# Kernel tuning notes

Hardware: AMD Instinct MI355X
Metric: run time of the kernel (lower is better)

The kernel has to match this reference:

```python
import jax, jax.numpy as jnp
import numpy as np

N_NODES = 100000
N_EDGES = 800000
DIMS = [(768, 64), (64, 32), (32, 16), (16, 5)]


def setup_inputs() -> dict:
    key = jax.random.key(0)
    ks = jax.random.split(key, 3 + 3 * len(DIMS))
    inp = {
        "x": jax.random.normal(ks[0], (N_NODES, DIMS[0][0]), jnp.float32),
        "edge_index": jax.random.randint(ks[1], (2, N_EDGES), 0, N_NODES),
        "edge_weight": jax.random.uniform(ks[2], (N_EDGES,), jnp.float32),
    }
    for i, (di, do) in enumerate(DIMS, start=1):
        s = 1.0 / np.sqrt(di)
        k0, k1, k2 = ks[3 * i], ks[3 * i + 1], ks[3 * i + 2]
        inp[f"W{i}l"] = jax.random.uniform(k0, (di, do), jnp.float32, -s, s)
        inp[f"W{i}r"] = jax.random.uniform(k1, (di, do), jnp.float32, -s, s)
        inp[f"b{i}"] = jax.random.uniform(k2, (do,), jnp.float32, -s, s)
    return inp


def _sage_conv(h, src, dst, inv_deg, Wl, Wr, b):
    # SAGEConv (mean aggregation): lin_l(mean_{j->i} h_j) + lin_r(h_i)
    agg = jax.ops.segment_sum(h[src], dst, num_segments=h.shape[0]) * inv_deg[:, None]
    return agg @ Wl + h @ Wr + b


def reference(x, edge_index, edge_weight,
              W1l, W1r, b1, W2l, W2r, b2, W3l, W3r, b3, W4l, W4r, b4):
    # edge_weight is accepted (matches original forward) but PyG SAGEConv mean
    # aggregation ignores it. Dropout is identity (deterministic eval reference).
    src, dst = edge_index[0], edge_index[1]
    deg = jax.ops.segment_sum(jnp.ones((src.shape[0],), x.dtype), dst,
                              num_segments=x.shape[0])
    inv_deg = jnp.where(deg > 0, 1.0 / deg, 0.0)
    h = jax.nn.relu(_sage_conv(x, src, dst, inv_deg, W1l, W1r, b1))
    h = jax.nn.relu(_sage_conv(h, src, dst, inv_deg, W2l, W2r, b2))
    h = jax.nn.relu(_sage_conv(h, src, dst, inv_deg, W3l, W3r, b3))
    return _sage_conv(h, src, dst, inv_deg, W4l, W4r, b4)
```

## Files before the change

kernel.cpp:

```cpp
#include <hip/hip_runtime.h>

using half8 = __attribute__((ext_vector_type(8))) _Float16;
using f32x4 = __attribute__((ext_vector_type(4))) float;

typedef __attribute__((address_space(3))) unsigned int lds_uint;
typedef __attribute__((address_space(1))) const unsigned int glb_uint;
__device__ __forceinline__ void async_copy16(const void* g, void* l) {
  __builtin_amdgcn_global_load_lds((glb_uint*)g, (lds_uint*)l, 16, 0, 0);
}

__device__ __forceinline__ void raw_barrier() {
  asm volatile("" ::: "memory");
  __builtin_amdgcn_s_barrier();
  asm volatile("" ::: "memory");
}

__global__ void zero_kernel(int4* __restrict__ p, int n4) {
  int i = blockIdx.x * 256 + threadIdx.x;
  if (i < n4) p[i] = make_int4(0, 0, 0, 0);
}

__global__ void prep_all_kernel(const float* __restrict__ W1l, const float* __restrict__ W1r,
                                const float* __restrict__ W2l, const float* __restrict__ W2r,
                                const float* __restrict__ W3l, const float* __restrict__ W3r,
                                const float* __restrict__ W4l, const float* __restrict__ W4r,
                                _Float16* __restrict__ w1, _Float16* __restrict__ w2,
                                _Float16* __restrict__ w3, _Float16* __restrict__ w4) {
  int i = blockIdx.x * 256 + threadIdx.x;
  if (i < 98304) {
    int c = i / 768, k = i - c * 768;
    float v = (c < 64) ? W1l[k * 64 + c] : W1r[k * 64 + (c - 64)];
    w1[i] = (_Float16)v;
  } else if (i < 98304 + 4096) {
    int j = i - 98304;
    int c = j >> 6, k = j & 63;
    float v = (c < 32) ? W2l[k * 32 + c] : W2r[k * 32 + (c - 32)];
    w2[j] = (_Float16)v;
  } else if (i < 98304 + 4096 + 1024) {
    int j = i - (98304 + 4096);
    int c = j >> 5, k = j & 31;
    float v = (c < 16) ? W3l[k * 16 + c] : W3r[k * 16 + (c - 16)];
    w3[j] = (_Float16)v;
  } else if (i < 98304 + 4096 + 1024 + 512) {
    int j = i - (98304 + 4096 + 1024);
    int c = j >> 5, k = j & 31;
    float v = 0.f;
    if (k < 16) {
      if (c < 5) v = W4l[k * 5 + c];
      else if (c < 10) v = W4r[k * 5 + (c - 5)];
    }
    w4[j] = (_Float16)v;
  }
}

__global__ void deg_kernel(const int* __restrict__ dst, int* __restrict__ cnt, int e) {
  int i = blockIdx.x * 256 + threadIdx.x;
  if (i < e) atomicAdd(&cnt[dst[i]], 1);
}

__global__ void scan1_kernel(const int* __restrict__ cnt, int* __restrict__ off,
                             int* __restrict__ bsum, float* __restrict__ invd, int nodes) {
  __shared__ int sh[256];
  int tid = threadIdx.x;
  int base = blockIdx.x * 1024 + tid * 4;
  int a0 = (base + 0 < nodes) ? cnt[base + 0] : 0;
  int a1 = (base + 1 < nodes) ? cnt[base + 1] : 0;
  int a2 = (base + 2 < nodes) ? cnt[base + 2] : 0;
  int a3 = (base + 3 < nodes) ? cnt[base + 3] : 0;
  if (base + 0 < nodes) invd[base + 0] = a0 > 0 ? 1.0f / (float)a0 : 0.f;
  if (base + 1 < nodes) invd[base + 1] = a1 > 0 ? 1.0f / (float)a1 : 0.f;
  if (base + 2 < nodes) invd[base + 2] = a2 > 0 ? 1.0f / (float)a2 : 0.f;
  if (base + 3 < nodes) invd[base + 3] = a3 > 0 ? 1.0f / (float)a3 : 0.f;
  int s3 = a0 + a1 + a2 + a3;
  sh[tid] = s3;
  __syncthreads();
  for (int d = 1; d < 256; d <<= 1) {
    int v = (tid >= d) ? sh[tid - d] : 0;
    __syncthreads();
    sh[tid] += v;
    __syncthreads();
  }
  int excl = sh[tid] - s3;
  if (base + 0 <= nodes) off[base + 0] = excl;
  if (base + 1 <= nodes) off[base + 1] = excl + a0;
  if (base + 2 <= nodes) off[base + 2] = excl + a0 + a1;
  if (base + 3 <= nodes) off[base + 3] = excl + a0 + a1 + a2;
  if (tid == 255) bsum[blockIdx.x] = sh[255];
}

__global__ void scan2_kernel(int* __restrict__ bsum, int nb) {
  __shared__ int sh[128];
  int tid = threadIdx.x;
  int v = (tid < nb) ? bsum[tid] : 0;
  sh[tid] = v;
  __syncthreads();
  for (int d = 1; d < 128; d <<= 1) {
    int u = (tid >= d) ? sh[tid - d] : 0;
    __syncthreads();
    sh[tid] += u;
    __syncthreads();
  }
  if (tid < nb) bsum[tid] = sh[tid] - v;
}

__global__ void scan3_kernel(int* __restrict__ off, const int* __restrict__ bsum, int ntot) {
  int i = blockIdx.x * 256 + threadIdx.x;
  if (i < ntot) off[i] += bsum[i >> 10];
}

__global__ void sortfill_kernel(const int* __restrict__ src, const int* __restrict__ dst,
                                const int* __restrict__ off, int* __restrict__ cur,
                                int* __restrict__ csr, int e) {
  int i = blockIdx.x * 256 + threadIdx.x;
  if (i < e) {
    int d = dst[i];
    int pos = atomicAdd(&cur[d], 1);
    csr[off[d] + pos] = src[i];
  }
}

__global__ __launch_bounds__(256, 3) void gemm1_kernel(
    const float* __restrict__ x,
    const _Float16* __restrict__ w16,
    const float* __restrict__ bias,
    _Float16* __restrict__ p, _Float16* __restrict__ q, int n) {
  constexpr int DI = 768, BK = 32, NT = DI / BK;
  __shared__ float aS[2][128 * BK];
  __shared__ _Float16 bS[2][128 * BK];
  int t = threadIdx.x;
  int lane = t & 63, w = t >> 6;
  int lm = lane & 15, lk = lane >> 4;
  int m0 = blockIdx.x * 128;

  const float* agp[4];
  int abase[4];
#pragma unroll
  for (int j = 0; j < 4; ++j) {
    int g = (j * 4 + w) * 64 + lane;
    int row = g >> 3, gi = g & 7;
    int gj = gi ^ (row & 7);
    int grow = m0 + row;
    if (grow >= n) grow = n - 1;
    agp[j] = x + (size_t)grow * DI + gj * 4;
    abase[j] = (j * 4 + w) * 256;
  }
  const _Float16* bgp[2];
  int bbase[2];
#pragma unroll
  for (int j = 0; j < 2; ++j) {
    int g = (j * 4 + w) * 64 + lane;
    int c = g >> 2, gi = g & 3;
    int gj = gi ^ ((c >> 1) & 3);
    bgp[j] = w16 + (size_t)c * DI + gj * 8;
    bbase[j] = (j * 4 + w) * 512;
  }

  f32x4 acc[2][8];
#pragma unroll
  for (int mi = 0; mi < 2; ++mi)
#pragma unroll
    for (int ni = 0; ni < 8; ++ni) acc[mi][ni] = (f32x4){0.f, 0.f, 0.f, 0.f};

  int r0l = w * 32 + lm, r1l = r0l + 16;
  int sw = lm & 7;
  int bsw = (lk ^ ((lm >> 1) & 3)) << 3;

  auto compute_tile = [&](const float* ab, const _Float16* bb) {
    f32x4 v0a = *(const f32x4*)(ab + r0l * 32 + (((lk * 2 + 0) ^ sw) << 2));
    f32x4 v0b = *(const f32x4*)(ab + r0l * 32 + (((lk * 2 + 1) ^ sw) << 2));
    f32x4 v1a = *(const f32x4*)(ab + r1l * 32 + (((lk * 2 + 0) ^ sw) << 2));
    f32x4 v1b = *(const f32x4*)(ab + r1l * 32 + (((lk * 2 + 1) ^ sw) << 2));
    half8 a0, a1;
#pragma unroll
    for (int j = 0; j < 4; ++j) {
      a0[j] = (_Float16)v0a[j]; a0[4 + j] = (_Float16)v0b[j];
      a1[j] = (_Float16)v1a[j]; a1[4 + j] = (_Float16)v1b[j];
    }
#pragma unroll
    for (int ni = 0; ni < 8; ++ni) {
      half8 b = *(const half8*)(bb + ni * 512 + lm * 32 + bsw);
      acc[0][ni] = __builtin_amdgcn_mfma_f32_16x16x32_f16(a0, b, acc[0][ni], 0, 0, 0);
      acc[1][ni] = __builtin_amdgcn_mfma_f32_16x16x32_f16(a1, b, acc[1][ni], 0, 0, 0);
    }
  };

#pragma unroll
  for (int j = 0; j < 4; ++j) async_copy16(agp[j], &aS[0][abase[j]]);
#pragma unroll
  for (int j = 0; j < 2; ++j) async_copy16(bgp[j], &bS[0][bbase[j]]);

  for (int ts = 0; ts < NT - 1; ++ts) {
    int cur = ts & 1;
    int kc = (ts + 1) * BK;
#pragma unroll
    for (int j = 0; j < 4; ++j) async_copy16(agp[j] + kc, &aS[cur ^ 1][abase[j]]);
#pragma unroll
    for (int j = 0; j < 2; ++j) async_copy16(bgp[j] + kc, &bS[cur ^ 1][bbase[j]]);
    asm volatile("s_waitcnt vmcnt(6)" ::: "memory");
    raw_barrier();
    compute_tile(aS[cur], bS[cur]);
    raw_barrier();
  }
  asm volatile("s_waitcnt vmcnt(0)" ::: "memory");
  raw_barrier();
  compute_tile(aS[(NT - 1) & 1], bS[(NT - 1) & 1]);

#pragma unroll
  for (int mi = 0; mi < 2; ++mi)
#pragma unroll
    for (int ni = 0; ni < 8; ++ni) {
      int col = ni * 16 + lm;
#pragma unroll
      for (int j = 0; j < 4; ++j) {
        int row = m0 + w * 32 + mi * 16 + lk * 4 + j;
        if (row < n) {
          float v = acc[mi][ni][j];
          if (col < 64) p[(size_t)row * 64 + col] = (_Float16)v;
          else q[(size_t)row * 64 + (col - 64)] = (_Float16)(v + bias[col - 64]);
        }
      }
    }
}

template <int DIR, int DIP, int PSI, int NC, int NCR, int DO, int PSO>
__global__ __launch_bounds__(256) void fused_agg_gemm_kernel(
    const _Float16* __restrict__ pin, const _Float16* __restrict__ qin,
    const int* __restrict__ off, const int* __restrict__ csr, const float* __restrict__ invd,
    const _Float16* __restrict__ w16, const float* __restrict__ bias,
    _Float16* __restrict__ pout, _Float16* __restrict__ qout, int n) {
  constexpr int SP = DIP + 8;
  constexpr int C8 = DIR / 8;
  constexpr int CT = C8 / 2;
  constexpr int NF = NC / 16;
  __shared__ _Float16 hs[128 * SP];
  int t = threadIdx.x;
  int node_l = t >> 1, half = t & 1;
  int node = blockIdx.x * 128 + node_l;

  if (node < n) {
    int e0 = off[node], e1 = off[node + 1];
    const half8* p8 = (const half8*)pin;
    float s[CT][8];
#pragma unroll
    for (int c = 0; c < CT; ++c)
#pragma unroll
      for (int j = 0; j < 8; ++j) s[c][j] = 0.f;
    for (int e = e0; e < e1; ++e) {
      int src = csr[e];
#pragma unroll
      for (int c = 0; c < CT; ++c) {
        half8 v = p8[(size_t)src * PSI + half * CT + c];
#pragma unroll
        for (int j = 0; j < 8; ++j) s[c][j] += (float)v[j];
      }
    }
    float id = invd[node];
#pragma unroll
    for (int c = 0; c < CT; ++c) {
      half8 qv = ((const half8*)qin)[(size_t)node * PSI + half * CT + c];
      half8 o;
#pragma unroll
      for (int j = 0; j < 8; ++j) o[j] = (_Float16)fmaxf(s[c][j] * id + (float)qv[j], 0.f);
      *(half8*)(hs + node_l * SP + (half * CT + c) * 8) = o;
    }
    if (DIP > DIR) {
      half8 z = {};
      *(half8*)(hs + node_l * SP + (C8 + half) * 8) = z;
    }
  }
  __syncthreads();

  int lane = t & 63, w = t >> 6;
  int lm = lane & 15, lk = lane >> 4;
  int r0l = w * 32 + lm, r1l = r0l + 16;
  const _Float16* wp = w16 + (size_t)lm * DIP + lk * 8;
  f32x4 acc[2][NF];
#pragma unroll
  for (int mi = 0; mi < 2; ++mi)
#pragma unroll
    for (int ni = 0; ni < NF; ++ni) acc[mi][ni] = (f32x4){0.f, 0.f, 0.f, 0.f};
#pragma unroll
  for (int kc = 0; kc < DIP; kc += 32) {
    half8 a0 = *(const half8*)(hs + r0l * SP + kc + lk * 8);
    half8 a1 = *(const half8*)(hs + r1l * SP + kc + lk * 8);
#pragma unroll
    for (int ni = 0; ni < NF; ++ni) {
      half8 b = *(const half8*)(wp + (size_t)ni * 16 * DIP + kc);
      acc[0][ni] = __builtin_amdgcn_mfma_f32_16x16x32_f16(a0, b, acc[0][ni], 0, 0, 0);
      acc[1][ni] = __builtin_amdgcn_mfma_f32_16x16x32_f16(a1, b, acc[1][ni], 0, 0, 0);
    }
  }
#pragma unroll
  for (int mi = 0; mi < 2; ++mi)
#pragma unroll
    for (int ni = 0; ni < NF; ++ni) {
      int col = ni * 16 + lm;
      if (col >= NCR) continue;
#pragma unroll
      for (int j = 0; j < 4; ++j) {
        int row = blockIdx.x * 128 + w * 32 + mi * 16 + lk * 4 + j;
        if (row < n) {
          float v = acc[mi][ni][j];
          if (col < DO) pout[(size_t)row * PSO + col] = (_Float16)v;
          else qout[(size_t)row * PSO + (col - DO)] = (_Float16)(v + bias[col - DO]);
        }
      }
    }
}

__global__ __launch_bounds__(256) void aggregate_last_kernel(
    const _Float16* __restrict__ p, const _Float16* __restrict__ q,
    const int* __restrict__ off, const int* __restrict__ csr,
    const float* __restrict__ invd, float* __restrict__ out, int n) {
  int t = blockIdx.x * 256 + threadIdx.x;
  int node = t >> 3;
  int c = t & 7;
  if (node >= n || c >= 5) return;
  int e0 = off[node], e1 = off[node + 1];
  float s = 0.f;
  for (int e = e0; e < e1; ++e) s += (float)p[(size_t)csr[e] * 8 + c];
  out[(size_t)node * 5 + c] = s * invd[node] + (float)q[(size_t)node * 8 + c];
}

extern "C" void kernel_launch(void* const* d_in, const int* in_sizes, int n_in,
                              void* d_out, int out_size, void* d_ws, size_t ws_size,
                              hipStream_t stream) {
  const float* x = (const float*)d_in[0];
  const int* ei = (const int*)d_in[1];
  const int E = in_sizes[1] / 2;
  const int* esrc = ei;
  const int* edst = ei + E;
  const float* W1l = (const float*)d_in[3];
  const float* W1r = (const float*)d_in[4];
  const float* b1 = (const float*)d_in[5];
  const float* W2l = (const float*)d_in[6];
  const float* W2r = (const float*)d_in[7];
  const float* b2 = (const float*)d_in[8];
  const float* W3l = (const float*)d_in[9];
  const float* W3r = (const float*)d_in[10];
  const float* b3 = (const float*)d_in[11];
  const float* W4l = (const float*)d_in[12];
  const float* W4r = (const float*)d_in[13];
  const float* b4 = (const float*)d_in[14];
  const int N = in_sizes[0] / 768;
  float* out = (float*)d_out;
  (void)n_in; (void)out_size; (void)ws_size;

  char* base = (char*)d_ws;
  size_t o = 0;
  auto alloc = [&](size_t bytes) -> void* {
    void* ptr = base + o;
    o = (o + bytes + 255) & ~(size_t)255;
    return ptr;
  };
  int* cnt = (int*)alloc((size_t)2 * N * 4);
  int* cur = cnt + N;
  int* off = (int*)alloc((size_t)(N + 1) * 4);
  int* bsum = (int*)alloc(1024);
  int* csr = (int*)alloc((size_t)E * 4);
  float* invd = (float*)alloc((size_t)N * 4);
  _Float16* w1 = (_Float16*)alloc((size_t)128 * 768 * 2);
  _Float16* w2 = (_Float16*)alloc((size_t)64 * 64 * 2);
  _Float16* w3 = (_Float16*)alloc((size_t)32 * 32 * 2);
  _Float16* w4 = (_Float16*)alloc((size_t)16 * 32 * 2);
  _Float16* P1 = (_Float16*)alloc((size_t)N * 64 * 2);
  _Float16* Q1 = (_Float16*)alloc((size_t)N * 64 * 2);
  _Float16* P2 = (_Float16*)alloc((size_t)N * 32 * 2);
  _Float16* Q2 = (_Float16*)alloc((size_t)N * 32 * 2);
  _Float16* P3 = (_Float16*)alloc((size_t)N * 16 * 2);
  _Float16* Q3 = (_Float16*)alloc((size_t)N * 16 * 2);
  _Float16* P4 = (_Float16*)alloc((size_t)N * 8 * 2);
  _Float16* Q4 = (_Float16*)alloc((size_t)N * 8 * 2);

  const int n4 = (2 * N + 3) / 4;
  zero_kernel<<<(n4 + 255) / 256, 256, 0, stream>>>((int4*)cnt, n4);
  prep_all_kernel<<<(98304 + 4096 + 1024 + 512 + 255) / 256, 256, 0, stream>>>(
      W1l, W1r, W2l, W2r, W3l, W3r, W4l, W4r, w1, w2, w3, w4);

  deg_kernel<<<(E + 255) / 256, 256, 0, stream>>>(edst, cnt, E);
  const int nb = (N + 1 + 1023) / 1024;
  scan1_kernel<<<nb, 256, 0, stream>>>(cnt, off, bsum, invd, N);
  scan2_kernel<<<1, 128, 0, stream>>>(bsum, nb);
  scan3_kernel<<<(N + 1 + 255) / 256, 256, 0, stream>>>(off, bsum, N + 1);
  sortfill_kernel<<<(E + 255) / 256, 256, 0, stream>>>(esrc, edst, off, cur, csr, E);

  const int gb = (N + 127) / 128;
  gemm1_kernel<<<gb, 256, 0, stream>>>(x, w1, b1, P1, Q1, N);
  fused_agg_gemm_kernel<64, 64, 8, 64, 64, 32, 32>
      <<<gb, 256, 0, stream>>>(P1, Q1, off, csr, invd, w2, b2, P2, Q2, N);
  fused_agg_gemm_kernel<32, 32, 4, 32, 32, 16, 16>
      <<<gb, 256, 0, stream>>>(P2, Q2, off, csr, invd, w3, b3, P3, Q3, N);
  fused_agg_gemm_kernel<16, 32, 2, 16, 10, 5, 8>
      <<<gb, 256, 0, stream>>>(P3, Q3, off, csr, invd, w4, b4, P4, Q4, N);
  aggregate_last_kernel<<<(N * 8 + 255) / 256, 256, 0, stream>>>(P4, Q4, off, csr, invd, out, N);
}
```

Baseline: 269.8 us.

## Widen per-node aggregation threads, unroll edge loop, fuse zeroing into prep

Fuses the counter-zeroing kernel into the weight-prep kernel to save a launch. The fused aggregate+GEMM kernels move to 512-thread blocks with four threads per node. Each wave now does one 16-row MFMA tile, and edge gathers are unrolled by two to get more loads in flight. The final aggregation uses one thread per node with vectorised half8 loads instead of eight scalar-loading threads. This trades some per-thread work and occupancy changes for more memory-level parallelism in the latency-bound gathers.

```diff
diff --git a/kernel.cpp b/kernel.cpp
--- a/kernel.cpp
+++ b/kernel.cpp
@@ -15,17 +15,13 @@
   asm volatile("" ::: "memory");
 }
 
-__global__ void zero_kernel(int4* __restrict__ p, int n4) {
-  int i = blockIdx.x * 256 + threadIdx.x;
-  if (i < n4) p[i] = make_int4(0, 0, 0, 0);
-}
-
-__global__ void prep_all_kernel(const float* __restrict__ W1l, const float* __restrict__ W1r,
-                                const float* __restrict__ W2l, const float* __restrict__ W2r,
-                                const float* __restrict__ W3l, const float* __restrict__ W3r,
-                                const float* __restrict__ W4l, const float* __restrict__ W4r,
-                                _Float16* __restrict__ w1, _Float16* __restrict__ w2,
-                                _Float16* __restrict__ w3, _Float16* __restrict__ w4) {
+__global__ void prep_zero_kernel(const float* __restrict__ W1l, const float* __restrict__ W1r,
+                                 const float* __restrict__ W2l, const float* __restrict__ W2r,
+                                 const float* __restrict__ W3l, const float* __restrict__ W3r,
+                                 const float* __restrict__ W4l, const float* __restrict__ W4r,
+                                 _Float16* __restrict__ w1, _Float16* __restrict__ w2,
+                                 _Float16* __restrict__ w3, _Float16* __restrict__ w4,
+                                 int4* __restrict__ zp, int n4) {
   int i = blockIdx.x * 256 + threadIdx.x;
   if (i < 98304) {
     int c = i / 768, k = i - c * 768;
@@ -50,6 +46,9 @@
       else if (c < 10) v = W4r[k * 5 + (c - 5)];
     }
     w4[j] = (_Float16)v;
+  } else {
+    int j = i - (98304 + 4096 + 1024 + 512);
+    if (j < n4) zp[j] = make_int4(0, 0, 0, 0);
   }
 }
 
@@ -223,103 +222,133 @@
 }
 
 template <int DIR, int DIP, int PSI, int NC, int NCR, int DO, int PSO>
-__global__ __launch_bounds__(256) void fused_agg_gemm_kernel(
+__global__ __launch_bounds__(512) void fused_agg_gemm_kernel(
     const _Float16* __restrict__ pin, const _Float16* __restrict__ qin,
     const int* __restrict__ off, const int* __restrict__ csr, const float* __restrict__ invd,
     const _Float16* __restrict__ w16, const float* __restrict__ bias,
     _Float16* __restrict__ pout, _Float16* __restrict__ qout, int n) {
   constexpr int SP = DIP + 8;
   constexpr int C8 = DIR / 8;
-  constexpr int CT = C8 / 2;
+  constexpr int ACT = (C8 >= 4) ? 4 : C8;
+  constexpr int CQ = C8 / ACT;
   constexpr int NF = NC / 16;
   __shared__ _Float16 hs[128 * SP];
   int t = threadIdx.x;
-  int node_l = t >> 1, half = t & 1;
+  int node_l = t >> 2, q4 = t & 3;
   int node = blockIdx.x * 128 + node_l;
 
   if (node < n) {
-    int e0 = off[node], e1 = off[node + 1];
-    const half8* p8 = (const half8*)pin;
-    float s[CT][8];
-#pragma unroll
-    for (int c = 0; c < CT; ++c)
-#pragma unroll
-      for (int j = 0; j < 8; ++j) s[c][j] = 0.f;
-    for (int e = e0; e < e1; ++e) {
-      int src = csr[e];
-#pragma unroll
-      for (int c = 0; c < CT; ++c) {
-        half8 v = p8[(size_t)src * PSI + half * CT + c];
-#pragma unroll
-        for (int j = 0; j < 8; ++j) s[c][j] += (float)v[j];
+    if (q4 < ACT) {
+      int e0 = off[node], e1 = off[node + 1];
+      const half8* p8 = (const half8*)pin;
+      float s[CQ][8];
+#pragma unroll
+      for (int c = 0; c < CQ; ++c)
+#pragma unroll
+        for (int j = 0; j < 8; ++j) s[c][j] = 0.f;
+      int e = e0;
+      for (; e + 2 <= e1; e += 2) {
+        int i0 = csr[e], i1 = csr[e + 1];
+        half8 v0[CQ], v1[CQ];
+#pragma unroll
+        for (int c = 0; c < CQ; ++c) v0[c] = p8[(size_t)i0 * PSI + q4 * CQ + c];
+#pragma unroll
+        for (int c = 0; c < CQ; ++c) v1[c] = p8[(size_t)i1 * PSI + q4 * CQ + c];
+#pragma unroll
+        for (int c = 0; c < CQ; ++c)
+#pragma unroll
+          for (int j = 0; j < 8; ++j) {
+            s[c][j] += (float)v0[c][j];
+            s[c][j] += (float)v1[c][j];
+          }
       }
-    }
-    float id = invd[node];
-#pragma unroll
-    for (int c = 0; c < CT; ++c) {
-      half8 qv = ((const half8*)qin)[(size_t)node * PSI + half * CT + c];
-      half8 o;
-#pragma unroll
-      for (int j = 0; j < 8; ++j) o[j] = (_Float16)fmaxf(s[c][j] * id + (float)qv[j], 0.f);
-      *(half8*)(hs + node_l * SP + (half * CT + c) * 8) = o;
-    }
-    if (DIP > DIR) {
+      if (e < e1) {
+        int i0 = csr[e];
+#pragma unroll
+        for (int c = 0; c < CQ; ++c) {
+          half8 v = p8[(size_t)i0 * PSI + q4 * CQ + c];
+#pragma unroll
+          for (int j = 0; j < 8; ++j) s[c][j] += (float)v[j];
+        }
+      }
+      float id = invd[node];
+#pragma unroll
+      for (int c = 0; c < CQ; ++c) {
+        half8 qv = ((const half8*)qin)[(size_t)node * PSI + q4 * CQ + c];
+        half8 o;
+#pragma unroll
+        for (int j = 0; j < 8; ++j) o[j] = (_Float16)fmaxf(s[c][j] * id + (float)qv[j], 0.f);
+        *(half8*)(hs + node_l * SP + (q4 * CQ + c) * 8) = o;
+      }
+    } else if (DIP > DIR && (q4 - ACT) < (DIP - DIR) / 8) {
       half8 z = {};
-      *(half8*)(hs + node_l * SP + (C8 + half) * 8) = z;
+      *(half8*)(hs + node_l * SP + (C8 + (q4 - ACT)) * 8) = z;
     }
   }
   __syncthreads();
 
   int lane = t & 63, w = t >> 6;
   int lm = lane & 15, lk = lane >> 4;
-  int r0l = w * 32 + lm, r1l = r0l + 16;
+  int row_l = w * 16 + lm;
   const _Float16* wp = w16 + (size_t)lm * DIP + lk * 8;
-  f32x4 acc[2][NF];
-#pragma unroll
-  for (int mi = 0; mi < 2; ++mi)
-#pragma unroll
-    for (int ni = 0; ni < NF; ++ni) acc[mi][ni] = (f32x4){0.f, 0.f, 0.f, 0.f};
+  f32x4 acc[NF];
+#pragma unroll
+  for (int ni = 0; ni < NF; ++ni) acc[ni] = (f32x4){0.f, 0.f, 0.f, 0.f};
 #pragma unroll
   for (int kc = 0; kc < DIP; kc += 32) {
-    half8 a0 = *(const half8*)(hs + r0l * SP + kc + lk * 8);
-    half8 a1 = *(const half8*)(hs + r1l * SP + kc + lk * 8);
+    half8 a = *(const half8*)(hs + row_l * SP + kc + lk * 8);
 #pragma unroll
     for (int ni = 0; ni < NF; ++ni) {
       half8 b = *(const half8*)(wp + (size_t)ni * 16 * DIP + kc);
-      acc[0][ni] = __builtin_amdgcn_mfma_f32_16x16x32_f16(a0, b, acc[0][ni], 0, 0, 0);
-      acc[1][ni] = __builtin_amdgcn_mfma_f32_16x16x32_f16(a1, b, acc[1][ni], 0, 0, 0);
-    }
-  }
-#pragma unroll
-  for (int mi = 0; mi < 2; ++mi)
-#pragma unroll
-    for (int ni = 0; ni < NF; ++ni) {
-      int col = ni * 16 + lm;
-      if (col >= NCR) continue;
-#pragma unroll
-      for (int j = 0; j < 4; ++j) {
-        int row = blockIdx.x * 128 + w * 32 + mi * 16 + lk * 4 + j;
-        if (row < n) {
-          float v = acc[mi][ni][j];
-          if (col < DO) pout[(size_t)row * PSO + col] = (_Float16)v;
-          else qout[(size_t)row * PSO + (col - DO)] = (_Float16)(v + bias[col - DO]);
-        }
+      acc[ni] = __builtin_amdgcn_mfma_f32_16x16x32_f16(a, b, acc[ni], 0, 0, 0);
+    }
+  }
+#pragma unroll
+  for (int ni = 0; ni < NF; ++ni) {
+    int col = ni * 16 + lm;
+    if (col >= NCR) continue;
+#pragma unroll
+    for (int j = 0; j < 4; ++j) {
+      int row = blockIdx.x * 128 + w * 16 + lk * 4 + j;
+      if (row < n) {
+        float v = acc[ni][j];
+        if (col < DO) pout[(size_t)row * PSO + col] = (_Float16)v;
+        else qout[(size_t)row * PSO + (col - DO)] = (_Float16)(v + bias[col - DO]);
       }
     }
+  }
 }
 
 __global__ __launch_bounds__(256) void aggregate_last_kernel(
     const _Float16* __restrict__ p, const _Float16* __restrict__ q,
     const int* __restrict__ off, const int* __restrict__ csr,
     const float* __restrict__ invd, float* __restrict__ out, int n) {
-  int t = blockIdx.x * 256 + threadIdx.x;
-  int node = t >> 3;
-  int c = t & 7;
-  if (node >= n || c >= 5) return;
+  int node = blockIdx.x * 256 + threadIdx.x;
+  if (node >= n) return;
   int e0 = off[node], e1 = off[node + 1];
-  float s = 0.f;
-  for (int e = e0; e < e1; ++e) s += (float)p[(size_t)csr[e] * 8 + c];
-  out[(size_t)node * 5 + c] = s * invd[node] + (float)q[(size_t)node * 8 + c];
+  const half8* p8 = (const half8*)p;
+  float s[8];
+#pragma unroll
+  for (int j = 0; j < 8; ++j) s[j] = 0.f;
+  int e = e0;
+  for (; e + 2 <= e1; e += 2) {
+    half8 v0 = p8[csr[e]];
+    half8 v1 = p8[csr[e + 1]];
+#pragma unroll
+    for (int j = 0; j < 8; ++j) {
+      s[j] += (float)v0[j];
+      s[j] += (float)v1[j];
+    }
+  }
+  if (e < e1) {
+    half8 v = p8[csr[e]];
+#pragma unroll
+    for (int j = 0; j < 8; ++j) s[j] += (float)v[j];
+  }
+  float id = invd[node];
+  half8 qv = ((const half8*)q)[node];
+#pragma unroll
+  for (int j = 0; j < 5; ++j) out[(size_t)node * 5 + j] = s[j] * id + (float)qv[j];
 }
 
 extern "C" void kernel_launch(void* const* d_in, const int* in_sizes, int n_in,
@@ -373,9 +402,9 @@
   _Float16* Q4 = (_Float16*)alloc((size_t)N * 8 * 2);
 
   const int n4 = (2 * N + 3) / 4;
-  zero_kernel<<<(n4 + 255) / 256, 256, 0, stream>>>((int4*)cnt, n4);
-  prep_all_kernel<<<(98304 + 4096 + 1024 + 512 + 255) / 256, 256, 0, stream>>>(
-      W1l, W1r, W2l, W2r, W3l, W3r, W4l, W4r, w1, w2, w3, w4);
+  const int prep_tot = 98304 + 4096 + 1024 + 512 + n4;
+  prep_zero_kernel<<<(prep_tot + 255) / 256, 256, 0, stream>>>(
+      W1l, W1r, W2l, W2r, W3l, W3r, W4l, W4r, w1, w2, w3, w4, (int4*)cnt, n4);
 
   deg_kernel<<<(E + 255) / 256, 256, 0, stream>>>(edst, cnt, E);
   const int nb = (N + 1 + 1023) / 1024;
@@ -384,13 +413,13 @@
   scan3_kernel<<<(N + 1 + 255) / 256, 256, 0, stream>>>(off, bsum, N + 1);
   sortfill_kernel<<<(E + 255) / 256, 256, 0, stream>>>(esrc, edst, off, cur, csr, E);
 
+  gemm1_kernel<<<(N + 127) / 128, 256, 0, stream>>>(x, w1, b1, P1, Q1, N);
   const int gb = (N + 127) / 128;
-  gemm1_kernel<<<gb, 256, 0, stream>>>(x, w1, b1, P1, Q1, N);
   fused_agg_gemm_kernel<64, 64, 8, 64, 64, 32, 32>
-      <<<gb, 256, 0, stream>>>(P1, Q1, off, csr, invd, w2, b2, P2, Q2, N);
+      <<<gb, 512, 0, stream>>>(P1, Q1, off, csr, invd, w2, b2, P2, Q2, N);
   fused_agg_gemm_kernel<32, 32, 4, 32, 32, 16, 16>
-      <<<gb, 256, 0, stream>>>(P2, Q2, off, csr, invd, w3, b3, P3, Q3, N);
+      <<<gb, 512, 0, stream>>>(P2, Q2, off, csr, invd, w3, b3, P3, Q3, N);
   fused_agg_gemm_kernel<16, 32, 2, 16, 10, 5, 8>
-      <<<gb, 256, 0, stream>>>(P3, Q3, off, csr, invd, w4, b4, P4, Q4, N);
-  aggregate_last_kernel<<<(N * 8 + 255) / 256, 256, 0, stream>>>(P4, Q4, off, csr, invd, out, N);
-}
+      <<<gb, 512, 0, stream>>>(P3, Q3, off, csr, invd, w4, b4, P4, Q4, N);
+  aggregate_last_kernel<<<(N + 255) / 256, 256, 0, stream>>>(P4, Q4, off, csr, invd, out, N);
+}
```

After: 255.7 us. 5.2% less time.
